# Optimization experiments

Measured on AMD Instinct MI355X. Metric: run time of the kernel, lower is better.

The kernel has to match this reference:

```python
import jax, jax.numpy as jnp
import numpy as np

N_QUBITS = 7
DEPTH = 2
DIM = 2 ** N_QUBITS  # 128
BATCH = 262144

# Qiskit little-endian convention: statevector index bit q = (idx >> q) & 1.
_idx = np.arange(DIM)
_bits = (_idx[:, None] >> np.arange(N_QUBITS)) & 1            # (DIM, N_QUBITS)
# CZ on all adjacent pairs (q, q+1): sign = (-1)^sum(bit_q * bit_{q+1})
_cz_parity = np.sum(_bits[:, :-1] * _bits[:, 1:], axis=1) % 2
CZ_PHASE = jnp.asarray(1.0 - 2.0 * _cz_parity, dtype=jnp.float32)   # (DIM,)
# Z_i expectation signs: <Z_i> = sum_idx p(idx) * (1 - 2*bit_i)
Z_SIGNS = jnp.asarray(1.0 - 2.0 * _bits, dtype=jnp.float32)         # (DIM, N_QUBITS)


def _apply_ry(state, q, theta_q):
    # state: (B, DIM) real amplitudes; RY is real so state stays real.
    lo = 2 ** q
    hi = DIM // (2 * lo)
    s = state.reshape(-1, hi, 2, lo)
    half = theta_q * 0.5
    c, sn = jnp.cos(half), jnp.sin(half)
    a0, a1 = s[:, :, 0, :], s[:, :, 1, :]
    out = jnp.stack([c * a0 - sn * a1, sn * a0 + c * a1], axis=2)
    return out.reshape(-1, DIM)


def setup_inputs() -> dict:
    key = jax.random.key(0)
    k1, k2 = jax.random.split(key)
    embed = jax.random.normal(k1, (BATCH, DIM), dtype=jnp.float32)
    theta = jax.random.normal(k2, (DEPTH * N_QUBITS,), dtype=jnp.float32) * 0.1
    return {"embed": embed, "theta": theta}


def reference(embed, theta):
    # Amplitude encoding: L2-normalize each row.
    state = embed / jnp.linalg.norm(embed, axis=1, keepdims=True)
    for d in range(DEPTH):
        for q in range(N_QUBITS):
            state = _apply_ry(state, q, theta[d * N_QUBITS + q])
        state = state * CZ_PHASE[None, :]
    probs = state * state                  # (B, DIM)
    return probs @ Z_SIGNS                 # (B, N_QUBITS)
```

## Files before the change

kernel.cpp:

```cpp
#include <hip/hip_runtime.h>
#include <utility>

#define NQ   7
#define DIM  128

template<class F, int... I>
__device__ __forceinline__ void static_for_impl(F&& f, std::integer_sequence<int, I...>) {
    (f(std::integral_constant<int, I>{}), ...);
}
template<int N, class F>
__device__ __forceinline__ void static_for(F&& f) {
    static_for_impl(static_cast<F&&>(f), std::make_integer_sequence<int, N>{});
}

__global__ __launch_bounds__(64, 2)
void qnat_kernel(const float* __restrict__ embed,
                 const float* __restrict__ theta,
                 float* __restrict__ out)
{
    const int lane = threadIdx.x;
    const size_t row = (size_t)blockIdx.x * 64 + lane;
    const float4* __restrict__ g4 =
        reinterpret_cast<const float4*>(embed) + row * 32;

    float st[DIM];

    static_for<32>([&](auto J) {
        constexpr int j = J.value;
        const float4 v = g4[j];
        st[4 * j + 0] = v.x;
        st[4 * j + 1] = v.y;
        st[4 * j + 2] = v.z;
        st[4 * j + 3] = v.w;
    });

    float ss = 0.f;
    static_for<DIM>([&](auto I) {
        constexpr int i = I.value;
        ss = fmaf(st[i], st[i], ss);
    });

    static_for<2>([&](auto D) {
        constexpr int d = D.value;
        static_for<NQ>([&](auto Q) {
            constexpr int q = Q.value;
            const float half = 0.5f * theta[d * NQ + q];
            const float c_ = __cosf(half);
            const float s_ = __sinf(half);
            static_for<64>([&](auto P) {
                constexpr int p  = P.value;
                constexpr int lo = 1 << q;
                constexpr int i0 = ((p >> q) << (q + 1)) | (p & (lo - 1));
                constexpr int i1 = i0 | lo;
                const float a0 = st[i0], a1 = st[i1];
                st[i0] = fmaf(c_, a0, -s_ * a1);
                st[i1] = fmaf(s_, a0,  c_ * a1);
            });
        });
        static_for<DIM>([&](auto I) {
            constexpr int i = I.value;
            constexpr int par = __builtin_popcount(i & (i >> 1)) & 1;
            if constexpr (par) st[i] = -st[i];
        });
    });

    static_for<DIM>([&](auto I) {
        constexpr int i = I.value;
        st[i] *= st[i];
    });

    float o[NQ];
    static_for<NQ>([&](auto K) {
        constexpr int k = K.value;
        constexpr int n = DIM >> (k + 1);
        float acc = 0.f;
        static_for<64>([&](auto I) {
            constexpr int i = I.value;
            if constexpr (i < n) {
                const float a = st[2 * i], b = st[2 * i + 1];
                acc += a - b;
                st[i] = a + b;
            }
        });
        o[k] = acc;
    });

    const float invss = __builtin_amdgcn_rcpf(ss);
    static_for<NQ>([&](auto K) { o[K.value] *= invss; });

    __shared__ float lds[64 * NQ];
    static_for<NQ>([&](auto K) {
        constexpr int k = K.value;
        lds[lane * NQ + k] = o[k];
    });
    __syncthreads();
    float* __restrict__ ob = out + (size_t)blockIdx.x * (64 * NQ);
    static_for<NQ>([&](auto K) {
        constexpr int k = K.value;
        ob[k * 64 + lane] = lds[k * 64 + lane];
    });
}

extern "C" void kernel_launch(void* const* d_in, const int* in_sizes, int n_in,
                              void* d_out, int out_size, void* d_ws, size_t ws_size,
                              hipStream_t stream)
{
    const float* embed = (const float*)d_in[0];
    const float* theta = (const float*)d_in[1];
    float* out = (float*)d_out;
    const int batch = in_sizes[0] / DIM;
    dim3 grid(batch / 64), block(64);
    hipLaunchKernelGGL(qnat_kernel, grid, block, 0, stream, embed, theta, out);
}
```

Measured before the change: 202.9 us.

## Coalesce embed loads through padded LDS transpose with software prefetch

Before, each lane loaded its own 512-byte row, so a wavefront's float4 loads were strided by 512 bytes. Now 8 lanes cooperatively load contiguous 128-byte chunks of 8 rows each, stage them in a padded LDS tile, and each lane reads back its own row's 32 floats per chunk. The next chunk is prefetched into registers while the current one is transposed. This makes global loads coalesced but adds LDS traffic, eight barriers and extra register pressure for the prefetch buffers.

Result: slower. 241.8 us (+19.2%).

```diff
diff --git a/kernel.cpp b/kernel.cpp
--- a/kernel.cpp
+++ b/kernel.cpp
@@ -18,20 +18,48 @@
                  const float* __restrict__ theta,
                  float* __restrict__ out)
 {
+    __shared__ float4 lds4[64 * 9];
     const int lane = threadIdx.x;
-    const size_t row = (size_t)blockIdx.x * 64 + lane;
+    const size_t rowBase = (size_t)blockIdx.x * 64;
     const float4* __restrict__ g4 =
-        reinterpret_cast<const float4*>(embed) + row * 32;
+        reinterpret_cast<const float4*>(embed) + rowBase * 32;
+    const int gr = lane >> 3;
+    const int gq = lane & 7;
 
     float st[DIM];
+    float4 cur[8];
 
-    static_for<32>([&](auto J) {
+    static_for<8>([&](auto J) {
         constexpr int j = J.value;
-        const float4 v = g4[j];
-        st[4 * j + 0] = v.x;
-        st[4 * j + 1] = v.y;
-        st[4 * j + 2] = v.z;
-        st[4 * j + 3] = v.w;
+        cur[j] = g4[(size_t)(j * 8 + gr) * 32 + gq];
+    });
+
+    static_for<4>([&](auto C) {
+        constexpr int c = C.value;
+        float4 nxt[8];
+        if constexpr (c < 3) {
+            static_for<8>([&](auto J) {
+                constexpr int j = J.value;
+                nxt[j] = g4[(size_t)(j * 8 + gr) * 32 + (c + 1) * 8 + gq];
+            });
+        }
+        static_for<8>([&](auto J) {
+            constexpr int j = J.value;
+            lds4[(j * 8 + gr) * 9 + gq] = cur[j];
+        });
+        __syncthreads();
+        static_for<8>([&](auto J) {
+            constexpr int j = J.value;
+            const float4 v = lds4[lane * 9 + j];
+            st[c * 32 + 4 * j + 0] = v.x;
+            st[c * 32 + 4 * j + 1] = v.y;
+            st[c * 32 + 4 * j + 2] = v.z;
+            st[c * 32 + 4 * j + 3] = v.w;
+        });
+        __syncthreads();
+        if constexpr (c < 3) {
+            static_for<8>([&](auto J) { cur[J.value] = nxt[J.value]; });
+        }
     });
 
     float ss = 0.f;
@@ -59,8 +87,7 @@
         });
         static_for<DIM>([&](auto I) {
             constexpr int i = I.value;
-            constexpr int par = __builtin_popcount(i & (i >> 1)) & 1;
-            if constexpr (par) st[i] = -st[i];
+            if constexpr (__builtin_popcount(i & (i >> 1)) & 1) st[i] = -st[i];
         });
     });
 
@@ -88,16 +115,17 @@
     const float invss = __builtin_amdgcn_rcpf(ss);
     static_for<NQ>([&](auto K) { o[K.value] *= invss; });
 
-    __shared__ float lds[64 * NQ];
+    float* ldsf = reinterpret_cast<float*>(lds4);
+    __syncthreads();
     static_for<NQ>([&](auto K) {
         constexpr int k = K.value;
-        lds[lane * NQ + k] = o[k];
+        ldsf[lane * NQ + k] = o[k];
     });
     __syncthreads();
     float* __restrict__ ob = out + (size_t)blockIdx.x * (64 * NQ);
     static_for<NQ>([&](auto K) {
         constexpr int k = K.value;
-        ob[k * 64 + lane] = lds[k * 64 + lane];
+        ob[k * 64 + lane] = ldsf[k * 64 + lane];
     });
 }
 
```

## Split each statevector across two lanes with DPP exchange and coalesced LDS staging

Applied to the files above, without the earlier changes.

Each row is now handled by a pair of lanes, each holding 64 amplitudes, so 32 rows map to one 64-thread block. The top-qubit RY gate and the reductions use DPP adjacent-lane swaps instead of per-thread work. Input is loaded with coalesced float4 reads into a padded LDS tile, replacing per-thread strided row loads. This halves register pressure per thread and doubles thread count, which should improve occupancy and memory coalescing. The cost is extra LDS traffic, a second barrier and the cross-lane operations.

Result: faster. 193.0 us (-4.8%).

```diff
diff --git a/kernel.cpp b/kernel.cpp
--- a/kernel.cpp
+++ b/kernel.cpp
@@ -3,6 +3,8 @@
 
 #define NQ   7
 #define DIM  128
+#define HALF 64
+#define RPB  32
 
 template<class F, int... I>
 __device__ __forceinline__ void static_for_impl(F&& f, std::integer_sequence<int, I...>) {
@@ -13,21 +15,36 @@
     static_for_impl(static_cast<F&&>(f), std::make_integer_sequence<int, N>{});
 }
 
+__device__ __forceinline__ float swap_adj(float x) {
+    int v = __builtin_amdgcn_update_dpp(0, __builtin_bit_cast(int, x),
+                                        0xB1 ,
+                                        0xF, 0xF, true);
+    return __builtin_bit_cast(float, v);
+}
+
 __global__ __launch_bounds__(64, 2)
 void qnat_kernel(const float* __restrict__ embed,
                  const float* __restrict__ theta,
                  float* __restrict__ out)
 {
+    __shared__ float4 tile[RPB * 33];
     const int lane = threadIdx.x;
-    const size_t row = (size_t)blockIdx.x * 64 + lane;
+    const int t = lane >> 1;
+    const int h = lane & 1;
     const float4* __restrict__ g4 =
-        reinterpret_cast<const float4*>(embed) + row * 32;
+        reinterpret_cast<const float4*>(embed) + (size_t)blockIdx.x * (RPB * 32);
 
-    float st[DIM];
+    static_for<16>([&](auto J) {
+        constexpr int j = J.value;
+        const float4 v = g4[j * 64 + lane];
+        tile[(2 * j + (lane >> 5)) * 33 + (lane & 31)] = v;
+    });
+    __syncthreads();
 
-    static_for<32>([&](auto J) {
+    float st[HALF];
+    static_for<16>([&](auto J) {
         constexpr int j = J.value;
-        const float4 v = g4[j];
+        const float4 v = tile[t * 33 + h * 16 + j];
         st[4 * j + 0] = v.x;
         st[4 * j + 1] = v.y;
         st[4 * j + 2] = v.z;
@@ -35,19 +52,21 @@
     });
 
     float ss = 0.f;
-    static_for<DIM>([&](auto I) {
+    static_for<HALF>([&](auto I) {
         constexpr int i = I.value;
         ss = fmaf(st[i], st[i], ss);
     });
+    ss += swap_adj(ss);
+
+    const float hs = h ? -1.f : 1.f;
 
     static_for<2>([&](auto D) {
         constexpr int d = D.value;
-        static_for<NQ>([&](auto Q) {
+        static_for<6>([&](auto Q) {
             constexpr int q = Q.value;
-            const float half = 0.5f * theta[d * NQ + q];
-            const float c_ = __cosf(half);
-            const float s_ = __sinf(half);
-            static_for<64>([&](auto P) {
+            const float ha = 0.5f * theta[d * NQ + q];
+            const float c_ = __cosf(ha), s_ = __sinf(ha);
+            static_for<32>([&](auto P) {
                 constexpr int p  = P.value;
                 constexpr int lo = 1 << q;
                 constexpr int i0 = ((p >> q) << (q + 1)) | (p & (lo - 1));
@@ -57,24 +76,34 @@
                 st[i1] = fmaf(s_, a0,  c_ * a1);
             });
         });
-        static_for<DIM>([&](auto I) {
-            constexpr int i = I.value;
-            constexpr int par = __builtin_popcount(i & (i >> 1)) & 1;
-            if constexpr (par) st[i] = -st[i];
+        {
+            const float ha = 0.5f * theta[d * NQ + 6];
+            const float c_ = __cosf(ha), s_ = __sinf(ha);
+            const float sgn = h ? s_ : -s_;
+            static_for<HALF>([&](auto J) {
+                constexpr int j = J.value;
+                const float other = swap_adj(st[j]);
+                st[j] = fmaf(sgn, other, c_ * st[j]);
+            });
+        }
+        static_for<HALF>([&](auto J) {
+            constexpr int j = J.value;
+            if constexpr ((__builtin_popcount(j & (j >> 1)) & 1) == 1) st[j] = -st[j];
+            if constexpr (((j >> 5) & 1) == 1) st[j] *= hs;
         });
     });
 
-    static_for<DIM>([&](auto I) {
-        constexpr int i = I.value;
-        st[i] *= st[i];
+    static_for<HALF>([&](auto J) {
+        constexpr int j = J.value;
+        st[j] *= st[j];
     });
 
     float o[NQ];
-    static_for<NQ>([&](auto K) {
+    static_for<6>([&](auto K) {
         constexpr int k = K.value;
-        constexpr int n = DIM >> (k + 1);
+        constexpr int n = HALF >> (k + 1);
         float acc = 0.f;
-        static_for<64>([&](auto I) {
+        static_for<32>([&](auto I) {
             constexpr int i = I.value;
             if constexpr (i < n) {
                 const float a = st[2 * i], b = st[2 * i + 1];
@@ -84,20 +113,35 @@
         });
         o[k] = acc;
     });
-
+    static_for<6>([&](auto K) {
+        constexpr int k = K.value;
+        o[k] += swap_adj(o[k]);
+    });
+    {
+        const float part = st[0];
+        o[6] = hs * (part - swap_adj(part));
+    }
     const float invss = __builtin_amdgcn_rcpf(ss);
     static_for<NQ>([&](auto K) { o[K.value] *= invss; });
 
-    __shared__ float lds[64 * NQ];
-    static_for<NQ>([&](auto K) {
-        constexpr int k = K.value;
-        lds[lane * NQ + k] = o[k];
-    });
     __syncthreads();
-    float* __restrict__ ob = out + (size_t)blockIdx.x * (64 * NQ);
-    static_for<NQ>([&](auto K) {
-        constexpr int k = K.value;
-        ob[k * 64 + lane] = lds[k * 64 + lane];
+    float* ldsf = reinterpret_cast<float*>(tile);
+    if (h == 0) {
+        static_for<NQ>([&](auto K) {
+            constexpr int k = K.value;
+            ldsf[t * NQ + k] = o[k];
+        });
+    }
+    __syncthreads();
+    float* __restrict__ ob = out + (size_t)blockIdx.x * (RPB * NQ);
+    static_for<4>([&](auto It) {
+        constexpr int it = It.value;
+        const int idx = it * 64 + lane;
+        if constexpr (it < 3) {
+            ob[idx] = ldsf[idx];
+        } else {
+            if (idx < RPB * NQ) ob[idx] = ldsf[idx];
+        }
     });
 }
 
@@ -109,6 +153,6 @@
     const float* theta = (const float*)d_in[1];
     float* out = (float*)d_out;
     const int batch = in_sizes[0] / DIM;
-    dim3 grid(batch / 64), block(64);
+    dim3 grid(batch / RPB), block(64);
     hipLaunchKernelGGL(qnat_kernel, grid, block, 0, stream, embed, theta, out);
 }
```
